# Optimization experiments

Measured on AMD Instinct MI355X. Metric: run time of the kernel, lower is better.

Reference implementation:

```python
import jax, jax.numpy as jnp
import numpy as np
import math

V, D, H, L, F, S, B = 32000, 1024, 16, 4, 4096, 1024, 2
DK = D // H
EPS = 1e-5


def _pe(seq_len, d_model):
    pos = jnp.arange(seq_len, dtype=jnp.float32)[:, None]
    div = jnp.exp(jnp.arange(0, d_model, 2, dtype=jnp.float32) * (-math.log(10000.0) / d_model))
    ang = pos * div  # [S, D/2]
    return jnp.stack([jnp.sin(ang), jnp.cos(ang)], axis=-1).reshape(seq_len, d_model)


def _ln(x, g, b):
    m = jnp.mean(x, axis=-1, keepdims=True)
    v = jnp.mean(jnp.square(x - m), axis=-1, keepdims=True)
    return (x - m) * jax.lax.rsqrt(v + EPS) * g + b


def setup_inputs() -> dict:
    key = jax.random.key(0)
    ks = jax.random.split(key, 12)
    std = 0.02
    inp = {
        "input_ids": jax.random.randint(ks[0], (B, S), 0, V, dtype=jnp.int32),
        "embed": std * jax.random.normal(ks[1], (V, D), dtype=jnp.float32),
        "Wq": std * jax.random.normal(ks[2], (L, D, D), dtype=jnp.float32),
        "bq": jnp.zeros((L, D), jnp.float32),
        "Wk": std * jax.random.normal(ks[3], (L, D, D), dtype=jnp.float32),
        "bk": jnp.zeros((L, D), jnp.float32),
        "Wv": std * jax.random.normal(ks[4], (L, D, D), dtype=jnp.float32),
        "bv": jnp.zeros((L, D), jnp.float32),
        "Wo": std * jax.random.normal(ks[5], (L, D, D), dtype=jnp.float32),
        "bo": jnp.zeros((L, D), jnp.float32),
        "ln1_g": jnp.ones((L, D), jnp.float32), "ln1_b": jnp.zeros((L, D), jnp.float32),
        "W1": std * jax.random.normal(ks[6], (L, F, D), dtype=jnp.float32),
        "b1": jnp.zeros((L, F), jnp.float32),
        "W2": std * jax.random.normal(ks[7], (L, D, F), dtype=jnp.float32),
        "b2": jnp.zeros((L, D), jnp.float32),
        "ln2_g": jnp.ones((L, D), jnp.float32), "ln2_b": jnp.zeros((L, D), jnp.float32),
        "lnf_g": jnp.ones((D,), jnp.float32), "lnf_b": jnp.zeros((D,), jnp.float32),
        "head_w": std * jax.random.normal(ks[8], (V, D), dtype=jnp.float32),
    }
    return inp


def _forward(input_ids, embed, Wq, bq, Wk, bk, Wv, bv, Wo, bo,
             ln1_g, ln1_b, W1, b1, W2, b2, ln2_g, ln2_b, lnf_g, lnf_b, head_w):
    b, s = input_ids.shape
    x = embed[input_ids] * jnp.float32(math.sqrt(D))  # [B,S,D]
    x = x + _pe(s, D)[None, :, :]
    causal = jnp.tril(jnp.ones((s, s), dtype=bool))  # [S,S]
    scale = jnp.float32(1.0 / math.sqrt(DK))
    for l in range(L):
        q = (x @ Wq[l].T + bq[l]).reshape(b, s, H, DK).transpose(0, 2, 1, 3)
        k = (x @ Wk[l].T + bk[l]).reshape(b, s, H, DK).transpose(0, 2, 1, 3)
        v = (x @ Wv[l].T + bv[l]).reshape(b, s, H, DK).transpose(0, 2, 1, 3)
        scores = jnp.einsum('bhqd,bhkd->bhqk', q, k) * scale
        scores = jnp.where(causal[None, None], scores, jnp.float32(-1e9))
        attn = jax.nn.softmax(scores, axis=-1)
        o = jnp.einsum('bhqk,bhkd->bhqd', attn, v).transpose(0, 2, 1, 3).reshape(b, s, D)
        o = o @ Wo[l].T + bo[l]
        x = _ln(x + o, ln1_g[l], ln1_b[l])
        ff = jax.nn.relu(x @ W1[l].T + b1[l]) @ W2[l].T + b2[l]
        x = _ln(x + ff, ln2_g[l], ln2_b[l])
    x = _ln(x, lnf_g, lnf_b)
    return x @ head_w.T  # logits [B,S,V]


def reference(input_ids, embed, Wq, bq, Wk, bk, Wv, bv, Wo, bo,
              ln1_g, ln1_b, W1, b1, W2, b2, ln2_g, ln2_b, lnf_g, lnf_b, head_w):
    return _forward(input_ids, embed, Wq, bq, Wk, bk, Wv, bv, Wo, bo,
                    ln1_g, ln1_b, W1, b1, W2, b2, ln2_g, ln2_b, lnf_g, lnf_b, head_w)
```

## Files before the change

kernel.cpp:

```cpp
#include <hip/hip_runtime.h>
#include <math.h>


namespace {
constexpr int kV  = 32000;
constexpr int kD  = 1024;
constexpr int kH  = 16;
constexpr int kL  = 4;
constexpr int kF  = 4096;
constexpr int kS  = 1024;
constexpr int kB  = 2;
constexpr int kDK = 64;
constexpr int kM  = kB * kS;
constexpr float kEps   = 1e-5f;
constexpr float kScale = 0.125f;
}

using short8 = __attribute__((ext_vector_type(8))) short;
using f32x4  = __attribute__((ext_vector_type(4))) float;

__device__ __forceinline__ unsigned short f2bf(float f) {
  union { float f; unsigned int u; } x{f};
  const unsigned int r = x.u + 0x7fffu + ((x.u >> 16) & 1u);
  return (unsigned short)(r >> 16);
}

__device__ __forceinline__ void llds16(const void* g, void* l) {
  __builtin_amdgcn_global_load_lds(
      (const __attribute__((address_space(1))) unsigned int*)g,
      (__attribute__((address_space(3))) unsigned int*)l, 16, 0, 0);
}

__device__ __forceinline__ float block_sum256(float v, float* scratch) {
#pragma unroll
  for (int off = 32; off > 0; off >>= 1) v += __shfl_down(v, off, 64);
  const int wid  = threadIdx.x >> 6;
  const int lane = threadIdx.x & 63;
  __syncthreads();
  if (lane == 0) scratch[wid] = v;
  __syncthreads();
  return scratch[0] + scratch[1] + scratch[2] + scratch[3];
}

__global__ __launch_bounds__(256) void f2bf_kernel(const float* __restrict__ in,
                                                   unsigned short* __restrict__ out,
                                                   int n4) {
  const int i = blockIdx.x * 256 + threadIdx.x;
  if (i < n4) {
    const float4 v = ((const float4*)in)[i];
    ushort4 o;
    o.x = f2bf(v.x); o.y = f2bf(v.y); o.z = f2bf(v.z); o.w = f2bf(v.w);
    ((ushort4*)out)[i] = o;
  }
}

__global__ __launch_bounds__(256) void embed_pe_kernel(
    const int* __restrict__ ids, const float* __restrict__ embed,
    float* __restrict__ x, unsigned short* __restrict__ xb) {
  const int row = blockIdx.x;
  const int s   = row & (kS - 1);
  const int id  = ids[row];
  const float* erow = embed + (size_t)id * kD;
#pragma unroll
  for (int i = 0; i < kD / 256; ++i) {
    const int d = threadIdx.x + i * 256;
    const int p = d >> 1;
    const double div = exp((double)(2 * p) * (-9.210340371976184 / 1024.0));
    const double ang = (double)s * div;
    const float pe = (d & 1) ? (float)cos(ang) : (float)sin(ang);
    const float v = erow[d] * 32.0f + pe;
    x[(size_t)row * kD + d]  = v;
    xb[(size_t)row * kD + d] = f2bf(v);
  }
}

template <int MODE>
__device__ __forceinline__ void gemm_core(int bm, int bn,
                                          const unsigned short* __restrict__ A,
                                          const unsigned short* __restrict__ W,
                                          const float* __restrict__ bias,
                                          void* __restrict__ Cout,
                                          int M, int N, int K,
                                          int k0begin, int k0end, float oscale) {
  __shared__ __align__(16) unsigned short As[128 * 32];
  __shared__ __align__(16) unsigned short Ws[128 * 32];
  const int t    = threadIdx.x;
  const int lane = t & 63;
  const int w    = t >> 6;
  const int wm   = (w >> 1) * 64;
  const int wn   = (w & 1) * 64;
  const int l15  = lane & 15;
  const int quad = lane >> 4;

  f32x4 acc[4][4] = {};

  for (int k0 = k0begin; k0 < k0end; k0 += 32) {
    __syncthreads();
#pragma unroll
    for (int i = 0; i < 2; ++i) {
      const int e   = i * 256 + t;
      const int row = e >> 2;
      const int kc  = (e & 3) * 8;
      const int ldsoff = (i * 256 + w * 64) * 8;
      llds16(A + (size_t)(bm + row) * K + k0 + kc, &As[ldsoff]);
      llds16(W + (size_t)(bn + row) * K + k0 + kc, &Ws[ldsoff]);
    }
    __syncthreads();
    short8 af[4], bf[4];
#pragma unroll
    for (int i = 0; i < 4; ++i)
      af[i] = *(const short8*)&As[(wm + i * 16 + l15) * 32 + quad * 8];
#pragma unroll
    for (int j = 0; j < 4; ++j)
      bf[j] = *(const short8*)&Ws[(wn + j * 16 + l15) * 32 + quad * 8];
#pragma unroll
    for (int i = 0; i < 4; ++i)
#pragma unroll
      for (int j = 0; j < 4; ++j)
        acc[i][j] = __builtin_amdgcn_mfma_f32_16x16x32_bf16(af[i], bf[j], acc[i][j], 0, 0, 0);
  }

#pragma unroll
  for (int i = 0; i < 4; ++i) {
#pragma unroll
    for (int r = 0; r < 4; ++r) {
      const int m = bm + wm + i * 16 + quad * 4 + r;
#pragma unroll
      for (int j = 0; j < 4; ++j) {
        const int n = bn + wn + j * 16 + l15;
        float v = acc[i][j][r] + (bias ? bias[n] : 0.0f);
        if (MODE == 2) v = fmaxf(v, 0.0f);
        if (MODE == 0) {
          ((float*)Cout)[(size_t)m * N + n] = v;
        } else if (MODE == 1) {
          const int b = m >> 10, s = m & 1023;
          const int h = n >> 6,  dk = n & 63;
          ((unsigned short*)Cout)[((size_t)(b * kH + h) * kS + s) * kDK + dk] = f2bf(v * oscale);
        } else if (MODE == 3) {
          const int b = m >> 10, s = m & 1023;
          const int h = n >> 6,  dk = n & 63;
          ((unsigned short*)Cout)[((size_t)(b * kH + h) * kDK + dk) * kS + s] = f2bf(v);
        } else {
          ((unsigned short*)Cout)[(size_t)m * N + n] = f2bf(v);
        }
      }
    }
  }
}

__global__ __launch_bounds__(256) void gemm_head_kernel(
    const unsigned short* __restrict__ A, const unsigned short* __restrict__ W,
    float* __restrict__ C) {
  const int bid = blockIdx.x;
  const int bm  = (bid & 15) * 128;
  const int bn  = (bid >> 4) * 128;
  gemm_core<0>(bm, bn, A, W, nullptr, C, kM, kV, kD, 0, kD, 1.0f);
}

__global__ __launch_bounds__(256) void gemm_qkv_kernel(
    const unsigned short* __restrict__ A,
    const unsigned short* __restrict__ wq, const unsigned short* __restrict__ wk,
    const unsigned short* __restrict__ wv,
    const float* __restrict__ bq_, const float* __restrict__ bk_,
    const float* __restrict__ bv_,
    unsigned short* __restrict__ qo, unsigned short* __restrict__ ko,
    unsigned short* __restrict__ vo) {
  const int bm = blockIdx.y * 128;
  const int bn = blockIdx.x * 128;
  const int z  = blockIdx.z;
  if (z == 0) {
    gemm_core<1>(bm, bn, A, wq, bq_, qo, kM, kD, kD, 0, kD, kScale);
  } else if (z == 1) {
    gemm_core<1>(bm, bn, A, wk, bk_, ko, kM, kD, kD, 0, kD, 1.0f);
  } else {
    gemm_core<3>(bm, bn, A, wv, bv_, vo, kM, kD, kD, 0, kD, 1.0f);
  }
}

__global__ __launch_bounds__(256) void gemm_splitk_kernel(
    const unsigned short* __restrict__ A, const unsigned short* __restrict__ W,
    const float* __restrict__ bias, float* __restrict__ C0,
    float* __restrict__ C1, int M, int N, int K) {
  const int bm = blockIdx.y * 128;
  const int bn = blockIdx.x * 128;
  if (blockIdx.z == 0)
    gemm_core<0>(bm, bn, A, W, bias, C0, M, N, K, 0, K / 2, 1.0f);
  else
    gemm_core<0>(bm, bn, A, W, nullptr, C1, M, N, K, K / 2, K, 1.0f);
}

__global__ __launch_bounds__(256) void gemm_bf16relu_kernel(
    const unsigned short* __restrict__ A, const unsigned short* __restrict__ W,
    const float* __restrict__ bias, unsigned short* __restrict__ C,
    int M, int N, int K) {
  gemm_core<2>(blockIdx.y * 128, blockIdx.x * 128, A, W, bias, C, M, N, K, 0, K, 1.0f);
}

__global__ __launch_bounds__(256) void attn_mfma_kernel(
    const unsigned short* __restrict__ q, const unsigned short* __restrict__ k,
    const unsigned short* __restrict__ vt, unsigned short* __restrict__ ob) {
  const int bid = blockIdx.x;
  const int qt  = bid & 15;
  const int h   = (bid >> 4) & 15;
  const int b   = bid >> 8;
  const int q0  = qt * 64;

  __shared__ __align__(16) unsigned short Qs[64 * 64];
  __shared__ __align__(16) unsigned short Ks[64 * 64];
  __shared__ __align__(16) unsigned short Vs[64 * 64];
  __shared__ __align__(16) unsigned short Ps[4][16 * 64];

  const int t    = threadIdx.x;
  const int lane = t & 63;
  const int w    = t >> 6;
  const int l15  = lane & 15;
  const int quad = lane >> 4;

  const size_t base = (size_t)(b * kH + h) * kS * kDK;

#pragma unroll
  for (int i = 0; i < 2; ++i) {
    const int e   = i * 256 + t;
    const int row = e >> 3;
    const int g   = e & 7;
    llds16(q + base + (size_t)(q0 + row) * kDK + ((g ^ (row & 7)) * 8),
           &Qs[(i * 256 + w * 64) * 8]);
  }
  __syncthreads();

  short8 aq[2];
#pragma unroll
  for (int ks = 0; ks < 2; ++ks)
    aq[ks] = *(const short8*)&Qs[(w * 16 + l15) * 64 + (((ks * 4 + quad) ^ (l15 & 7)) * 8)];

  f32x4 acc_o[4] = {};
  float m[4]    = {-1e30f, -1e30f, -1e30f, -1e30f};
  float lsum[4] = {0.f, 0.f, 0.f, 0.f};

  for (int kt = 0; kt <= qt; ++kt) {
    __syncthreads();
#pragma unroll
    for (int i = 0; i < 2; ++i) {
      const int e   = i * 256 + t;
      const int row = e >> 3;
      const int g   = e & 7;
      llds16(k + base + (size_t)(kt * 64 + row) * kDK + ((g ^ (row & 7)) * 8),
             &Ks[(i * 256 + w * 64) * 8]);
      llds16(vt + base + (size_t)row * kS + kt * 64 + ((g ^ (row & 7)) * 8),
             &Vs[(i * 256 + w * 64) * 8]);
    }
    __syncthreads();

    f32x4 s[4] = {};
#pragma unroll
    for (int j = 0; j < 4; ++j) {
#pragma unroll
      for (int ks = 0; ks < 2; ++ks) {
        const short8 bk8 = *(const short8*)&Ks[(j * 16 + l15) * 64 +
                                               (((ks * 4 + quad) ^ (l15 & 7)) * 8)];
        s[j] = __builtin_amdgcn_mfma_f32_16x16x32_bf16(aq[ks], bk8, s[j], 0, 0, 0);
      }
    }

    if (kt == qt) {
      const int rb = w * 16 + quad * 4;
#pragma unroll
      for (int j = 0; j < 4; ++j) {
        const int kg = j * 16 + l15;
#pragma unroll
        for (int r = 0; r < 4; ++r)
          if (kg > rb + r) s[j][r] = -1e30f;
      }
    }

    float pm[4];
#pragma unroll
    for (int r = 0; r < 4; ++r)
      pm[r] = fmaxf(fmaxf(s[0][r], s[1][r]), fmaxf(s[2][r], s[3][r]));
#pragma unroll
    for (int off = 8; off > 0; off >>= 1)
#pragma unroll
      for (int r = 0; r < 4; ++r)
        pm[r] = fmaxf(pm[r], __shfl_xor(pm[r], off, 64));

    float alpha[4];
#pragma unroll
    for (int r = 0; r < 4; ++r) {
      const float mn = fmaxf(m[r], pm[r]);
      alpha[r] = __expf(m[r] - mn);
      m[r] = mn;
    }

    float rs[4] = {0.f, 0.f, 0.f, 0.f};
    unsigned short pb16[4][4];
#pragma unroll
    for (int j = 0; j < 4; ++j)
#pragma unroll
      for (int r = 0; r < 4; ++r) {
        const float e = __expf(s[j][r] - m[r]);
        rs[r] += e;
        pb16[j][r] = f2bf(e);
      }
#pragma unroll
    for (int off = 8; off > 0; off >>= 1)
#pragma unroll
      for (int r = 0; r < 4; ++r)
        rs[r] += __shfl_xor(rs[r], off, 64);
#pragma unroll
    for (int r = 0; r < 4; ++r) lsum[r] = lsum[r] * alpha[r] + rs[r];
#pragma unroll
    for (int jd = 0; jd < 4; ++jd)
#pragma unroll
      for (int r = 0; r < 4; ++r) acc_o[jd][r] *= alpha[r];

#pragma unroll
    for (int j = 0; j < 4; ++j)
#pragma unroll
      for (int r = 0; r < 4; ++r) {
        const int row = quad * 4 + r;
        const int col = j * 16 + l15;
        Ps[w][row * 64 + (((col >> 3) ^ (row & 7)) << 3) + (col & 7)] = pb16[j][r];
      }
    asm volatile("s_waitcnt lgkmcnt(0)" ::: "memory");
    __builtin_amdgcn_sched_barrier(0);

    short8 ap[2];
#pragma unroll
    for (int ks = 0; ks < 2; ++ks)
      ap[ks] = *(const short8*)&Ps[w][l15 * 64 + (((ks * 4 + quad) ^ (l15 & 7)) * 8)];

#pragma unroll
    for (int jd = 0; jd < 4; ++jd) {
#pragma unroll
      for (int ks = 0; ks < 2; ++ks) {
        const short8 bv8 = *(const short8*)&Vs[(jd * 16 + l15) * 64 +
                                               (((ks * 4 + quad) ^ (l15 & 7)) * 8)];
        acc_o[jd] = __builtin_amdgcn_mfma_f32_16x16x32_bf16(ap[ks], bv8, acc_o[jd], 0, 0, 0);
      }
    }
  }

  float inv[4];
#pragma unroll
  for (int r = 0; r < 4; ++r) inv[r] = 1.0f / lsum[r];
#pragma unroll
  for (int jd = 0; jd < 4; ++jd)
#pragma unroll
    for (int r = 0; r < 4; ++r) {
      const int qg = q0 + w * 16 + quad * 4 + r;
      ob[(size_t)(b * kS + qg) * kD + h * kDK + jd * 16 + l15] =
          f2bf(acc_o[jd][r] * inv[r]);
    }
}

__global__ __launch_bounds__(256) void add_ln_kernel(
    float* __restrict__ x, const float* __restrict__ res,
    const float* __restrict__ res2,
    const float* __restrict__ g, const float* __restrict__ bta,
    unsigned short* __restrict__ xb) {
  const int row = blockIdx.x;
  const int t   = threadIdx.x;
  __shared__ float scratch[4];
  float vals[4];
  float sum = 0.f;
  float* xrow = x + (size_t)row * kD;
#pragma unroll
  for (int i = 0; i < 4; ++i) {
    const int d = t + i * 256;
    float vv = xrow[d];
    if (res)  vv += res[(size_t)row * kD + d];
    if (res2) vv += res2[(size_t)row * kD + d];
    vals[i] = vv;
    sum += vv;
  }
  const float mean = block_sum256(sum, scratch) * (1.0f / kD);
  float vsum = 0.f;
#pragma unroll
  for (int i = 0; i < 4; ++i) {
    const float dd = vals[i] - mean;
    vsum += dd * dd;
  }
  const float var  = block_sum256(vsum, scratch) * (1.0f / kD);
  const float rstd = rsqrtf(var + kEps);
#pragma unroll
  for (int i = 0; i < 4; ++i) {
    const int d = t + i * 256;
    const float o = (vals[i] - mean) * rstd * g[d] + bta[d];
    xrow[d] = o;
    xb[(size_t)row * kD + d] = f2bf(o);
  }
}

extern "C" void kernel_launch(void* const* d_in, const int* in_sizes, int n_in,
                              void* d_out, int out_size, void* d_ws, size_t ws_size,
                              hipStream_t stream) {
  const int*   ids   = (const int*)  d_in[0];
  const float* embed = (const float*)d_in[1];
  const float* Wq    = (const float*)d_in[2];
  const float* bq    = (const float*)d_in[3];
  const float* Wk    = (const float*)d_in[4];
  const float* bk    = (const float*)d_in[5];
  const float* Wv    = (const float*)d_in[6];
  const float* bv    = (const float*)d_in[7];
  const float* Wo    = (const float*)d_in[8];
  const float* bo    = (const float*)d_in[9];
  const float* ln1g  = (const float*)d_in[10];
  const float* ln1b  = (const float*)d_in[11];
  const float* W1    = (const float*)d_in[12];
  const float* b1    = (const float*)d_in[13];
  const float* W2    = (const float*)d_in[14];
  const float* b2    = (const float*)d_in[15];
  const float* ln2g  = (const float*)d_in[16];
  const float* ln2b  = (const float*)d_in[17];
  const float* lnfg  = (const float*)d_in[18];
  const float* lnfb  = (const float*)d_in[19];
  const float* headw = (const float*)d_in[20];

  char* ws = (char*)d_ws;
  float*          x    = (float*)          (ws);
  unsigned short* xb   = (unsigned short*) (ws + 8388608);
  unsigned short* qbb  = (unsigned short*) (ws + 12582912);
  unsigned short* kbb  = (unsigned short*) (ws + 16777216);
  unsigned short* vtb  = (unsigned short*) (ws + 20971520);
  unsigned short* ob   = (unsigned short*) (ws + 25165824);
  unsigned short* ff1b = (unsigned short*) (ws + 29360128);
  float*          pb   = (float*)          (ws + 46137344);
  float*          pb2  = (float*)          (ws + 54525952);
  unsigned short* wbuf = (unsigned short*) (ws + 67108864);

  const dim3 blk(256);
  embed_pe_kernel<<<kM, blk, 0, stream>>>(ids, embed, x, xb);

  for (int l = 0; l < kL; ++l) {
    const size_t oD = (size_t)l * kD * kD;
    const size_t oF = (size_t)l * kF * kD;
    f2bf_kernel<<<1024, blk, 0, stream>>>(Wq + oD, wbuf,            262144);
    f2bf_kernel<<<1024, blk, 0, stream>>>(Wk + oD, wbuf + 1048576,  262144);
    f2bf_kernel<<<1024, blk, 0, stream>>>(Wv + oD, wbuf + 2097152,  262144);
    f2bf_kernel<<<1024, blk, 0, stream>>>(Wo + oD, wbuf + 3145728,  262144);
    f2bf_kernel<<<4096, blk, 0, stream>>>(W1 + oF, wbuf + 4194304, 1048576);
    f2bf_kernel<<<4096, blk, 0, stream>>>(W2 + oF, wbuf + 8388608, 1048576);

    gemm_qkv_kernel<<<dim3(8, 16, 3), blk, 0, stream>>>(
        xb, wbuf, wbuf + 1048576, wbuf + 2097152,
        bq + (size_t)l * kD, bk + (size_t)l * kD, bv + (size_t)l * kD,
        qbb, kbb, vtb);
    attn_mfma_kernel<<<kB * kH * (kS / 64), blk, 0, stream>>>(qbb, kbb, vtb, ob);
    gemm_splitk_kernel<<<dim3(8, 16, 2), blk, 0, stream>>>(
        ob, wbuf + 3145728, bo + (size_t)l * kD, pb, pb2, kM, kD, kD);
    add_ln_kernel<<<kM, blk, 0, stream>>>(
        x, pb, pb2, ln1g + (size_t)l * kD, ln1b + (size_t)l * kD, xb);
    gemm_bf16relu_kernel<<<dim3(32, 16), blk, 0, stream>>>(
        xb, wbuf + 4194304, b1 + (size_t)l * kF, ff1b, kM, kF, kD);
    gemm_splitk_kernel<<<dim3(8, 16, 2), blk, 0, stream>>>(
        ff1b, wbuf + 8388608, b2 + (size_t)l * kD, pb, pb2, kM, kD, kF);
    add_ln_kernel<<<kM, blk, 0, stream>>>(
        x, pb, pb2, ln2g + (size_t)l * kD, ln2b + (size_t)l * kD, xb);
  }

  add_ln_kernel<<<kM, blk, 0, stream>>>(x, nullptr, nullptr, lnfg, lnfb, xb);
  f2bf_kernel<<<32000, blk, 0, stream>>>(headw, wbuf, 8192000);
  gemm_head_kernel<<<dim3(4000), blk, 0, stream>>>(xb, wbuf, (float*)d_out);
}
```

Measured before the change: 1.579 ms.

## Fuse weight casts, drop attention LDS staging, remap blocks across XCDs, use float PE

Replaces the six per-layer weight-conversion launches with one fused kernel. Attention now reads Q, K and V^T fragments straight from global memory instead of staging them through LDS with barriers. The head GEMM and attention block indices are remapped so that consecutive blocks on the same XCD share data in L2. The positional encoding switches from double to float math. These save launch overhead and sync costs, but the direct global loads lose LDS reuse across waves, and float PE can drift slightly from the reference.

```diff
diff --git a/kernel.cpp b/kernel.cpp
--- a/kernel.cpp
+++ b/kernel.cpp
@@ -54,6 +54,31 @@
   }
 }
 
+__global__ __launch_bounds__(256) void f2bf_layer_kernel(
+    const float* __restrict__ wq, const float* __restrict__ wk,
+    const float* __restrict__ wv, const float* __restrict__ wo,
+    const float* __restrict__ w1, const float* __restrict__ w2,
+    unsigned short* __restrict__ dst) {
+  const int i = blockIdx.x * 256 + threadIdx.x;
+  const float* src;
+  size_t so, doff;
+  if (i < 1048576) {
+    const int seg = i >> 18;
+    const int off = i & 262143;
+    src = (seg == 0) ? wq : (seg == 1) ? wk : (seg == 2) ? wv : wo;
+    so = off;
+    doff = (size_t)seg * 1048576 + (size_t)off * 4;
+  } else {
+    const int j = i - 1048576;
+    if (j < 1048576) { src = w1; so = j; doff = 4194304 + (size_t)j * 4; }
+    else             { src = w2; so = j - 1048576; doff = 8388608 + (size_t)(j - 1048576) * 4; }
+  }
+  const float4 v = ((const float4*)src)[so];
+  ushort4 o;
+  o.x = f2bf(v.x); o.y = f2bf(v.y); o.z = f2bf(v.z); o.w = f2bf(v.w);
+  *(ushort4*)(dst + doff) = o;
+}
+
 __global__ __launch_bounds__(256) void embed_pe_kernel(
     const int* __restrict__ ids, const float* __restrict__ embed,
     float* __restrict__ x, unsigned short* __restrict__ xb) {
@@ -65,9 +90,9 @@
   for (int i = 0; i < kD / 256; ++i) {
     const int d = threadIdx.x + i * 256;
     const int p = d >> 1;
-    const double div = exp((double)(2 * p) * (-9.210340371976184 / 1024.0));
-    const double ang = (double)s * div;
-    const float pe = (d & 1) ? (float)cos(ang) : (float)sin(ang);
+    const float div = expf((float)p * -0.017988946039015984f);
+    const float ang = (float)s * div;
+    const float pe  = (d & 1) ? cosf(ang) : sinf(ang);
     const float v = erow[d] * 32.0f + pe;
     x[(size_t)row * kD + d]  = v;
     xb[(size_t)row * kD + d] = f2bf(v);
@@ -152,8 +177,9 @@
     const unsigned short* __restrict__ A, const unsigned short* __restrict__ W,
     float* __restrict__ C) {
   const int bid = blockIdx.x;
-  const int bm  = (bid & 15) * 128;
-  const int bn  = (bid >> 4) * 128;
+  const int wg  = (bid & 7) * 500 + (bid >> 3);
+  const int bm  = (wg & 15) * 128;
+  const int bn  = (wg >> 4) * 128;
   gemm_core<0>(bm, bn, A, W, nullptr, C, kM, kV, kD, 0, kD, 1.0f);
 }
 
@@ -200,14 +226,12 @@
     const unsigned short* __restrict__ q, const unsigned short* __restrict__ k,
     const unsigned short* __restrict__ vt, unsigned short* __restrict__ ob) {
   const int bid = blockIdx.x;
-  const int qt  = bid & 15;
-  const int h   = (bid >> 4) & 15;
-  const int b   = bid >> 8;
+  const int wg  = (bid & 7) * 64 + (bid >> 3);
+  const int qt  = wg & 15;
+  const int h   = (wg >> 4) & 15;
+  const int b   = wg >> 8;
   const int q0  = qt * 64;
 
-  __shared__ __align__(16) unsigned short Qs[64 * 64];
-  __shared__ __align__(16) unsigned short Ks[64 * 64];
-  __shared__ __align__(16) unsigned short Vs[64 * 64];
   __shared__ __align__(16) unsigned short Ps[4][16 * 64];
 
   const int t    = threadIdx.x;
@@ -218,46 +242,23 @@
 
   const size_t base = (size_t)(b * kH + h) * kS * kDK;
 
-#pragma unroll
-  for (int i = 0; i < 2; ++i) {
-    const int e   = i * 256 + t;
-    const int row = e >> 3;
-    const int g   = e & 7;
-    llds16(q + base + (size_t)(q0 + row) * kDK + ((g ^ (row & 7)) * 8),
-           &Qs[(i * 256 + w * 64) * 8]);
-  }
-  __syncthreads();
-
   short8 aq[2];
 #pragma unroll
   for (int ks = 0; ks < 2; ++ks)
-    aq[ks] = *(const short8*)&Qs[(w * 16 + l15) * 64 + (((ks * 4 + quad) ^ (l15 & 7)) * 8)];
+    aq[ks] = *(const short8*)(q + base + (size_t)(q0 + w * 16 + l15) * kDK + ks * 32 + quad * 8);
 
   f32x4 acc_o[4] = {};
   float m[4]    = {-1e30f, -1e30f, -1e30f, -1e30f};
   float lsum[4] = {0.f, 0.f, 0.f, 0.f};
 
   for (int kt = 0; kt <= qt; ++kt) {
-    __syncthreads();
-#pragma unroll
-    for (int i = 0; i < 2; ++i) {
-      const int e   = i * 256 + t;
-      const int row = e >> 3;
-      const int g   = e & 7;
-      llds16(k + base + (size_t)(kt * 64 + row) * kDK + ((g ^ (row & 7)) * 8),
-             &Ks[(i * 256 + w * 64) * 8]);
-      llds16(vt + base + (size_t)row * kS + kt * 64 + ((g ^ (row & 7)) * 8),
-             &Vs[(i * 256 + w * 64) * 8]);
-    }
-    __syncthreads();
-
     f32x4 s[4] = {};
 #pragma unroll
     for (int j = 0; j < 4; ++j) {
 #pragma unroll
       for (int ks = 0; ks < 2; ++ks) {
-        const short8 bk8 = *(const short8*)&Ks[(j * 16 + l15) * 64 +
-                                               (((ks * 4 + quad) ^ (l15 & 7)) * 8)];
+        const short8 bk8 = *(const short8*)(k + base +
+            (size_t)(kt * 64 + j * 16 + l15) * kDK + ks * 32 + quad * 8);
         s[j] = __builtin_amdgcn_mfma_f32_16x16x32_bf16(aq[ks], bk8, s[j], 0, 0, 0);
       }
     }
@@ -333,8 +334,8 @@
     for (int jd = 0; jd < 4; ++jd) {
 #pragma unroll
       for (int ks = 0; ks < 2; ++ks) {
-        const short8 bv8 = *(const short8*)&Vs[(jd * 16 + l15) * 64 +
-                                               (((ks * 4 + quad) ^ (l15 & 7)) * 8)];
+        const short8 bv8 = *(const short8*)(vt + base +
+            (size_t)(jd * 16 + l15) * kS + kt * 64 + ks * 32 + quad * 8);
         acc_o[jd] = __builtin_amdgcn_mfma_f32_16x16x32_bf16(ap[ks], bv8, acc_o[jd], 0, 0, 0);
       }
     }
@@ -434,12 +435,8 @@
   for (int l = 0; l < kL; ++l) {
     const size_t oD = (size_t)l * kD * kD;
     const size_t oF = (size_t)l * kF * kD;
-    f2bf_kernel<<<1024, blk, 0, stream>>>(Wq + oD, wbuf,            262144);
-    f2bf_kernel<<<1024, blk, 0, stream>>>(Wk + oD, wbuf + 1048576,  262144);
-    f2bf_kernel<<<1024, blk, 0, stream>>>(Wv + oD, wbuf + 2097152,  262144);
-    f2bf_kernel<<<1024, blk, 0, stream>>>(Wo + oD, wbuf + 3145728,  262144);
-    f2bf_kernel<<<4096, blk, 0, stream>>>(W1 + oF, wbuf + 4194304, 1048576);
-    f2bf_kernel<<<4096, blk, 0, stream>>>(W2 + oF, wbuf + 8388608, 1048576);
+    f2bf_layer_kernel<<<12288, blk, 0, stream>>>(
+        Wq + oD, Wk + oD, Wv + oD, Wo + oD, W1 + oF, W2 + oF, wbuf);
 
     gemm_qkv_kernel<<<dim3(8, 16, 3), blk, 0, stream>>>(
         xb, wbuf, wbuf + 1048576, wbuf + 2097152,
```

Result: slower. 1.651 ms (+4.6%).
